# Kernel optimization log

Hardware: AMD Instinct MI355X
Metric: run time of the kernel (lower is better)

The kernel has to match this reference:

```python
import jax, jax.numpy as jnp
import numpy as np

N_NODES = 50000
N_EDGES = 600000
NUM_ENTITIES = 50000
EMBED = 128
HIDDEN = 128
NUM_TYPES = 16


def setup_inputs() -> dict:
    key = jax.random.key(0)
    ks = jax.random.split(key, 12)
    entity = jax.random.randint(ks[0], (N_NODES,), 0, NUM_ENTITIES, dtype=jnp.int64 if jax.config.jax_enable_x64 else jnp.int32)
    edge_index = jax.random.randint(ks[1], (2, N_EDGES), 0, N_NODES, dtype=jnp.int32)
    s = 1.0 / np.sqrt(EMBED)
    emb = jax.random.normal(ks[2], (NUM_ENTITIES, EMBED), jnp.float32)
    emb = emb.at[0].set(0.0)  # padding_idx=0
    W1_l = jax.random.uniform(ks[3], (EMBED, HIDDEN), jnp.float32, -s, s)
    b1 = jax.random.uniform(ks[4], (HIDDEN,), jnp.float32, -s, s)
    W1_r = jax.random.uniform(ks[5], (EMBED, HIDDEN), jnp.float32, -s, s)
    W2_l = jax.random.uniform(ks[6], (HIDDEN, HIDDEN), jnp.float32, -s, s)
    b2 = jax.random.uniform(ks[7], (HIDDEN,), jnp.float32, -s, s)
    W2_r = jax.random.uniform(ks[8], (HIDDEN, HIDDEN), jnp.float32, -s, s)
    Wc = jax.random.uniform(ks[9], (HIDDEN, NUM_TYPES), jnp.float32, -s, s)
    bc = jax.random.uniform(ks[10], (NUM_TYPES,), jnp.float32, -s, s)
    return {"entity": entity, "edge_index": edge_index, "emb": emb,
            "W1_l": W1_l, "b1": b1, "W1_r": W1_r,
            "W2_l": W2_l, "b2": b2, "W2_r": W2_r,
            "Wc": Wc, "bc": bc}


def _sage_conv(x, src, dst, Wl, bl, Wr):
    # PyG SAGEConv (aggr='mean'): out = lin_l(mean_{j->i} x_j) + lin_r(x_i)
    msgs = x[src]                                            # [E, D] gather
    agg = jax.ops.segment_sum(msgs, dst, num_segments=N_NODES)
    deg = jax.ops.segment_sum(jnp.ones((src.shape[0],), x.dtype), dst, num_segments=N_NODES)
    agg = agg / jnp.maximum(deg, 1.0)[:, None]               # mean; 0 for isolated nodes
    return agg @ Wl + bl + x @ Wr


def reference(entity, edge_index, emb, W1_l, b1, W1_r, W2_l, b2, W2_r, Wc, bc):
    src, dst = edge_index[0], edge_index[1]
    x = emb[entity]                                          # [N, 128] embedding lookup
    x = jax.nn.relu(_sage_conv(x, src, dst, W1_l, b1, W1_r))
    x = _sage_conv(x, src, dst, W2_l, b2, W2_r)
    return x @ Wc + bc                                       # [N, num_node_types]
```

## Files before the change

kernel.cpp:

```cpp
#include <hip/hip_runtime.h>

typedef _Float16 half4  __attribute__((ext_vector_type(4)));
typedef _Float16 half8  __attribute__((ext_vector_type(8)));
typedef float    f32x4  __attribute__((ext_vector_type(4)));

#define EC 768
#define CAP 4096
#define CHUNK 2048
#define CPAD 16

__device__ __forceinline__ void gather_dev(const int* __restrict__ ent,
                                           const float* __restrict__ emb,
                                           _Float16* __restrict__ X, int gb, int N) {
  int t = gb * 256 + threadIdx.x;
  if (t >= N * 16) return;
  int node = t >> 4, g = t & 15;
  const float4* s = (const float4*)(emb + (long)ent[node] * 128 + g * 8);
  float4 a = s[0], c = s[1];
  half8 o;
  o[0] = (_Float16)a.x; o[1] = (_Float16)a.y; o[2] = (_Float16)a.z; o[3] = (_Float16)a.w;
  o[4] = (_Float16)c.x; o[5] = (_Float16)c.y; o[6] = (_Float16)c.z; o[7] = (_Float16)c.w;
  *(half8*)(X + (long)t * 8) = o;
}

__device__ __forceinline__ void pack_dev(const float* Wa, const float* Wb,
                                         _Float16* out, int NT, int ncols, int t) {
  int lane = t & 63, tile = t >> 6;
  int nt = tile % NT, kt = tile / NT;
  int n  = nt * 16 + (lane & 15);
  int kb = kt * 32 + (lane >> 4) * 8;
  half8 o;
#pragma unroll
  for (int j = 0; j < 8; ++j) {
    int k = kb + j;
    float w = (k < 128) ? Wa[k * ncols + n] : Wb[(k - 128) * ncols + n];
    o[j] = (_Float16)w;
  }
  *(half8*)(out + (long)t * 8) = o;
}

__global__ __launch_bounds__(256) void bucketA_k(
    const int* __restrict__ src, const int* __restrict__ dst,
    int* __restrict__ cur, int* __restrict__ buck,
    const int* __restrict__ ent, const float* __restrict__ emb, _Float16* __restrict__ X,
    const float* __restrict__ W1l, const float* __restrict__ W1r, _Float16* __restrict__ Wp1,
    const float* __restrict__ W2l, const float* __restrict__ W2r, const float* __restrict__ Wc,
    _Float16* __restrict__ Wz, const float* __restrict__ b2, const float* __restrict__ bc,
    float* __restrict__ bpr, int N, int E, int NA, int NBUCK, int ST, int IBA) {
  int b = blockIdx.x;
  if (b < IBA) {
    int grp = b / ST, ph = b % ST;
    if (ph != 0) { gather_dev(ent, emb, X, grp * (ST - 1) + ph - 1, N); return; }
    __shared__ int lbin[256], gbase[256];
    int tl = threadIdx.x;
    lbin[tl] = 0; __syncthreads();
    int e0 = grp * CHUNK;
    int pk[8], bn[8], lr[8];
    if (e0 + CHUNK <= E) {
      const int4* dp = (const int4*)(dst + e0 + tl * 8);
      const int4* sp = (const int4*)(src + e0 + tl * 8);
      int4 d0 = dp[0], d1 = dp[1], s0 = sp[0], s1 = sp[1];
      int dv[8] = {d0.x, d0.y, d0.z, d0.w, d1.x, d1.y, d1.z, d1.w};
      int sv[8] = {s0.x, s0.y, s0.z, s0.w, s1.x, s1.y, s1.z, s1.w};
#pragma unroll
      for (int k = 0; k < 8; ++k) {
        bn[k] = dv[k] >> 8;
        pk[k] = (sv[k] << 8) | (dv[k] & 255);
        lr[k] = atomicAdd(&lbin[bn[k]], 1);
      }
    } else {
#pragma unroll
      for (int k = 0; k < 8; ++k) {
        int e = e0 + tl * 8 + k;
        bn[k] = -1;
        if (e < E) {
          int d = dst[e];
          bn[k] = d >> 8;
          pk[k] = (src[e] << 8) | (d & 255);
          lr[k] = atomicAdd(&lbin[bn[k]], 1);
        }
      }
    }
    __syncthreads();
    gbase[tl] = (tl < NBUCK && lbin[tl]) ? atomicAdd(&cur[tl * CPAD], lbin[tl]) : 0;
    __syncthreads();
#pragma unroll
    for (int k = 0; k < 8; ++k) {
      if (bn[k] >= 0) {
        int idx = gbase[bn[k]] + lr[k];
        if (idx < CAP) buck[(long)bn[k] * CAP + idx] = pk[k];
      }
    }
  } else if (b < IBA + 16) {
    pack_dev(W1l, W1r, Wp1, 8, 128, (b - IBA) * 256 + threadIdx.x);
  } else if (b < IBA + 32) {
    int i = (b - IBA - 16) * 256 + threadIdx.x;
    int j = i & 7, lane = (i >> 3) & 63, tile = i >> 9;
    int nt = tile & 1, kt = tile >> 1;
    int k = kt * 32 + (lane >> 4) * 8 + j;
    int c = lane & 15;
    const float* W = nt ? W2r : W2l;
    float s = 0.f;
#pragma unroll 8
    for (int q = 0; q < 128; ++q) s += W[k * 128 + q] * Wc[q * 16 + c];
    Wz[i] = (_Float16)s;
  } else {
    int n = threadIdx.x;
    if (n < 16) {
      float s = bc[n];
      for (int k = 0; k < 128; ++k) s += b2[k] * Wc[k * 16 + n];
      bpr[n] = s;
    }
  }
}

__global__ __launch_bounds__(512) void bucketB_k(
    const int* __restrict__ cur, const int* __restrict__ buck,
    int* __restrict__ row_off, int* __restrict__ csr, int N, int E, int NBUCK) {
  int B0 = blockIdx.x, tl = threadIdx.x;
  __shared__ int sA[256], cnt[256], sB[256], run[256];
  if (tl < 256) sA[tl] = (tl < NBUCK) ? cur[tl * CPAD] : 0;
  if (tl < 256) cnt[tl] = 0;
  __syncthreads();
  for (int off = 1; off < 256; off <<= 1) {
    int a = (tl < 256) ? sA[tl] : 0;
    int bb = (tl >= off && tl < 256) ? sA[tl - off] : 0;
    __syncthreads();
    if (tl < 256) sA[tl] = a + bb;
    __syncthreads();
  }
  int bsz = cur[B0 * CPAD]; if (bsz > CAP) bsz = CAP;
  int ebase = sA[B0] - bsz;
  const int* bp = buck + (long)B0 * CAP;
  for (int i = tl; i < bsz; i += 512) atomicAdd(&cnt[bp[i] & 255], 1);
  __syncthreads();
  int cv = (tl < 256) ? cnt[tl] : 0;
  if (tl < 256) sB[tl] = cv;
  __syncthreads();
  for (int off = 1; off < 256; off <<= 1) {
    int a = (tl < 256) ? sB[tl] : 0;
    int bb = (tl >= off && tl < 256) ? sB[tl - off] : 0;
    __syncthreads();
    if (tl < 256) sB[tl] = a + bb;
    __syncthreads();
  }
  if (tl < 256) {
    int loff = sB[tl] - cv;
    int node = (B0 << 8) + tl;
    if (node < N) row_off[node] = ebase + loff;
    if (B0 == 0 && tl == 0) row_off[N] = E;
    run[tl] = loff;
  }
  __syncthreads();
  for (int i = tl; i < bsz; i += 512) {
    int w = bp[i];
    int r = atomicAdd(&run[w & 255], 1);
    csr[ebase + r] = w >> 8;
  }
}

__device__ __forceinline__ void agg_to_lds(const _Float16* __restrict__ X,
                                           const int* __restrict__ row_off,
                                           const int* __restrict__ csr,
                                           _Float16* ab, int* eidx,
                                           int row0, int M, int lane) {
  int nd_end = min(row0 + 16, M);
  int ebeg = row_off[row0 < M ? row0 : M - 1];
  int eend = row_off[nd_end];
  int cnt  = eend - ebeg;
  bool fits = (cnt <= EC);
  if (fits)
    for (int i = lane; i < cnt; i += 64) eidx[i] = csr[ebeg + i];
  int g = lane >> 4, j = lane & 15;
#pragma unroll
  for (int batch = 0; batch < 4; ++batch) {
    int node = row0 + batch * 4 + g;
    int nc = (node < M) ? node : M - 1;
    int beg = row_off[nc], end = row_off[nc + 1];
    half8 acc = (half8)(_Float16)0.f;
    if (fits) {
      const int* ix = eidx + (beg - ebeg);
      int n = end - beg;
#pragma unroll 8
      for (int e = 0; e < n; ++e) {
        half8 v = *(const half8*)(X + (long)ix[e] * 128 + j * 8);
        acc += v;
      }
    } else {
#pragma unroll 8
      for (int e = beg; e < end; ++e) {
        half8 v = *(const half8*)(X + (long)csr[e] * 128 + j * 8);
        acc += v;
      }
    }
    _Float16 inv = (_Float16)(1.f / fmaxf((float)(end - beg), 1.f));
    acc *= (half8)inv;
    *(half8*)(ab + (batch * 4 + g) * 136 + j * 8) = acc;
  }
}

__global__ __launch_bounds__(128) void gemm1z_k(const _Float16* __restrict__ X,
                                                const int* __restrict__ row_off,
                                                const int* __restrict__ csr,
                                                const _Float16* __restrict__ Bp,
                                                const float* __restrict__ bias,
                                                const _Float16* __restrict__ Bz,
                                                const float* __restrict__ bprime,
                                                _Float16* __restrict__ Zl,
                                                float* __restrict__ Pr, int M) {
  __shared__ _Float16 abuf[2][16 * 136];
  __shared__ int      ebuf[2][EC];
  int wave = threadIdx.x >> 6, lane = threadIdx.x & 63;
  _Float16* ab = abuf[wave];
  int row0 = blockIdx.x * 32 + wave * 16;
  agg_to_lds(X, row_off, csr, ab, ebuf[wave], row0, M, lane);
  int m = lane & 15, quad = lane >> 4;
  int arow = row0 + m; if (arow > M - 1) arow = M - 1;
  f32x4 acc[8];
#pragma unroll
  for (int i = 0; i < 8; ++i) acc[i] = (f32x4){0.f, 0.f, 0.f, 0.f};
#pragma unroll
  for (int kt = 0; kt < 8; ++kt) {
    half8 af = (kt < 4) ? *(const half8*)(ab + m * 136 + kt * 32 + quad * 8)
                        : *(const half8*)(X + (long)arow * 128 + (kt - 4) * 32 + quad * 8);
#pragma unroll
    for (int nt = 0; nt < 8; ++nt) {
      half8 bf = *(const half8*)(Bp + ((long)(kt * 8 + nt) * 64 + lane) * 8);
      acc[nt] = __builtin_amdgcn_mfma_f32_16x16x32_f16(af, bf, acc[nt], 0, 0, 0);
    }
  }
#pragma unroll
  for (int nt = 0; nt < 8; ++nt) {
    float bv = bias[nt * 16 + m];
#pragma unroll
    for (int r = 0; r < 4; ++r)
      ab[(quad * 4 + r) * 136 + nt * 16 + m] = (_Float16)fmaxf(acc[nt][r] + bv, 0.f);
  }
  f32x4 a0 = (f32x4){0.f, 0.f, 0.f, 0.f}, a1 = a0;
#pragma unroll
  for (int kt = 0; kt < 4; ++kt) {
    half8 af = *(const half8*)(ab + m * 136 + kt * 32 + quad * 8);
    half8 b0 = *(const half8*)(Bz + ((long)(kt * 2 + 0) * 64 + lane) * 8);
    half8 b1 = *(const half8*)(Bz + ((long)(kt * 2 + 1) * 64 + lane) * 8);
    a0 = __builtin_amdgcn_mfma_f32_16x16x32_f16(af, b0, a0, 0, 0, 0);
    a1 = __builtin_amdgcn_mfma_f32_16x16x32_f16(af, b1, a1, 0, 0, 0);
  }
  float bv = bprime[m];
#pragma unroll
  for (int r = 0; r < 4; ++r) {
    int orow = row0 + quad * 4 + r;
    if (orow < M) {
      Zl[(long)orow * 16 + m] = (_Float16)a0[r];
      Pr[(long)orow * 16 + m] = a1[r] + bv;
    }
  }
}

__global__ __launch_bounds__(256) void aggout_k(const _Float16* __restrict__ Zl,
                                                const float* __restrict__ Pr,
                                                const int* __restrict__ row_off,
                                                const int* __restrict__ csr,
                                                float* __restrict__ out, int M) {
  int t = blockIdx.x * 256 + threadIdx.x;
  int node = t >> 2, q = t & 3;
  if (node >= M) return;
  int beg = row_off[node], end = row_off[node + 1];
  float a0 = 0.f, a1 = 0.f, a2 = 0.f, a3 = 0.f;
#pragma unroll 8
  for (int e = beg; e < end; ++e) {
    half4 v = *(const half4*)(Zl + (long)csr[e] * 16 + q * 4);
    a0 += (float)v[0]; a1 += (float)v[1]; a2 += (float)v[2]; a3 += (float)v[3];
  }
  float inv = 1.f / fmaxf((float)(end - beg), 1.f);
  long o = (long)node * 16 + q * 4;
  const float4 pv = *(const float4*)(Pr + o);
  float4 ov;
  ov.x = a0 * inv + pv.x; ov.y = a1 * inv + pv.y;
  ov.z = a2 * inv + pv.z; ov.w = a3 * inv + pv.w;
  *(float4*)(out + o) = ov;
}

extern "C" void kernel_launch(void* const* d_in, const int* in_sizes, int n_in,
                              void* d_out, int out_size, void* d_ws, size_t ws_size,
                              hipStream_t stream) {
  const int N = in_sizes[0];
  const int E = in_sizes[1] / 2;
  const int*   entity = (const int*)d_in[0];
  const int*   e_src  = (const int*)d_in[1];
  const int*   e_dst  = e_src + E;
  const float* emb    = (const float*)d_in[2];
  const float* W1l    = (const float*)d_in[3];
  const float* b1     = (const float*)d_in[4];
  const float* W1r    = (const float*)d_in[5];
  const float* W2l    = (const float*)d_in[6];
  const float* b2     = (const float*)d_in[7];
  const float* W2r    = (const float*)d_in[8];
  const float* Wc     = (const float*)d_in[9];
  const float* bc     = (const float*)d_in[10];
  float* out = (float*)d_out;

  const int NBUCK = (N + 255) >> 8;

  char* p = (char*)d_ws;
  _Float16* x0  = (_Float16*)p; p += (size_t)N * 128 * 2;
  _Float16* Wp1 = (_Float16*)p; p += 256 * 128 * 2;
  _Float16* Wz  = (_Float16*)p; p += 128 * 32 * 2;
  float*    bpr = (float*)p;    p += 16 * 4;
  _Float16* Zl  = (_Float16*)p; p += (size_t)N * 16 * 2;
  float*    Pr  = (float*)p;    p += (size_t)N * 16 * 4;
  int* cur     = (int*)p; p += (size_t)NBUCK * CPAD * 4;
  int* row_off = (int*)p; p += (size_t)(N + 1) * 4;
  int* csr     = (int*)p; p += (size_t)E * 4;
  int* buck    = (int*)p; p += (size_t)NBUCK * CAP * 4;

  const int NA = (E + CHUNK - 1) / CHUNK;
  const int GB = (N * 16 + 255) / 256;
  const int GAper = (GB + NA - 1) / NA;
  const int ST  = GAper + 1;
  const int IBA = ST * NA;

  hipMemsetAsync(cur, 0, (size_t)NBUCK * CPAD * 4, stream);

  bucketA_k<<<IBA + 33, 256, 0, stream>>>(e_src, e_dst, cur, buck,
                                          entity, emb, x0, W1l, W1r, Wp1,
                                          W2l, W2r, Wc, Wz, b2, bc, bpr,
                                          N, E, NA, NBUCK, ST, IBA);
  bucketB_k<<<NBUCK, 512, 0, stream>>>(cur, buck, row_off, csr, N, E, NBUCK);
  gemm1z_k<<<(N + 31) / 32, 128, 0, stream>>>(x0, row_off, csr, Wp1, b1,
                                              Wz, bpr, Zl, Pr, N);
  aggout_k<<<(N * 4 + 255) / 256, 256, 0, stream>>>(Zl, Pr, row_off, csr, out, N);
}
```

Baseline: 162.4 us.

## Split embedding gather between bucketA and bucketB kernels to balance load

Caps the gather work co-scheduled with edge bucketing in the first kernel at four units per bucketing block. The remaining gather units move into extra blocks appended to the CSR-building kernel, which otherwise launches only a few hundred blocks. The aim is to shorten the first kernel and fill idle compute units during the second. The risk is that the extra blocks contend with the bucket blocks for bandwidth or delay them.

```diff
diff --git a/kernel.cpp b/kernel.cpp
--- a/kernel.cpp
+++ b/kernel.cpp
@@ -8,11 +8,13 @@
 #define CAP 4096
 #define CHUNK 2048
 #define CPAD 16
-
-__device__ __forceinline__ void gather_dev(const int* __restrict__ ent,
-                                           const float* __restrict__ emb,
-                                           _Float16* __restrict__ X, int gb, int N) {
-  int t = gb * 256 + threadIdx.x;
+#define GA_PER 4
+
+__device__ __forceinline__ void gather_unit(const int* __restrict__ ent,
+                                            const float* __restrict__ emb,
+                                            _Float16* __restrict__ X,
+                                            int unit, int lt, int N) {
+  int t = unit * 256 + lt;
   if (t >= N * 16) return;
   int node = t >> 4, g = t & 15;
   const float4* s = (const float4*)(emb + (long)ent[node] * 128 + g * 8);
@@ -46,11 +48,11 @@
     const float* __restrict__ W1l, const float* __restrict__ W1r, _Float16* __restrict__ Wp1,
     const float* __restrict__ W2l, const float* __restrict__ W2r, const float* __restrict__ Wc,
     _Float16* __restrict__ Wz, const float* __restrict__ b2, const float* __restrict__ bc,
-    float* __restrict__ bpr, int N, int E, int NA, int NBUCK, int ST, int IBA) {
+    float* __restrict__ bpr, int N, int E, int NA, int NBUCK, int IBA) {
   int b = blockIdx.x;
   if (b < IBA) {
-    int grp = b / ST, ph = b % ST;
-    if (ph != 0) { gather_dev(ent, emb, X, grp * (ST - 1) + ph - 1, N); return; }
+    int grp = b / (GA_PER + 1), ph = b % (GA_PER + 1);
+    if (ph != 0) { gather_unit(ent, emb, X, grp * GA_PER + ph - 1, threadIdx.x, N); return; }
     __shared__ int lbin[256], gbase[256];
     int tl = threadIdx.x;
     lbin[tl] = 0; __syncthreads();
@@ -116,8 +118,15 @@
 
 __global__ __launch_bounds__(512) void bucketB_k(
     const int* __restrict__ cur, const int* __restrict__ buck,
-    int* __restrict__ row_off, int* __restrict__ csr, int N, int E, int NBUCK) {
+    int* __restrict__ row_off, int* __restrict__ csr,
+    const int* __restrict__ ent, const float* __restrict__ emb,
+    _Float16* __restrict__ X, int goff, int N, int E, int NBUCK) {
   int B0 = blockIdx.x, tl = threadIdx.x;
+  if (B0 >= NBUCK) {
+    int unit = goff + (B0 - NBUCK) * 2 + (tl >> 8);
+    gather_unit(ent, emb, X, unit, tl & 255, N);
+    return;
+  }
   __shared__ int sA[256], cnt[256], sB[256], run[256];
   if (tl < 256) sA[tl] = (tl < NBUCK) ? cur[tl * CPAD] : 0;
   if (tl < 256) cnt[tl] = 0;
@@ -313,19 +322,21 @@
   int* csr     = (int*)p; p += (size_t)E * 4;
   int* buck    = (int*)p; p += (size_t)NBUCK * CAP * 4;
 
-  const int NA = (E + CHUNK - 1) / CHUNK;
-  const int GB = (N * 16 + 255) / 256;
-  const int GAper = (GB + NA - 1) / NA;
-  const int ST  = GAper + 1;
-  const int IBA = ST * NA;
+  const int NA  = (E + CHUNK - 1) / CHUNK;
+  const int GB  = (N * 16 + 255) / 256;
+  const int IBA = (GA_PER + 1) * NA;
+  int G1 = NA * GA_PER; if (G1 > GB) G1 = GB;
+  const int G2 = GB - G1;
+  const int BG = (G2 + 1) / 2;
 
   hipMemsetAsync(cur, 0, (size_t)NBUCK * CPAD * 4, stream);
 
   bucketA_k<<<IBA + 33, 256, 0, stream>>>(e_src, e_dst, cur, buck,
                                           entity, emb, x0, W1l, W1r, Wp1,
                                           W2l, W2r, Wc, Wz, b2, bc, bpr,
-                                          N, E, NA, NBUCK, ST, IBA);
-  bucketB_k<<<NBUCK, 512, 0, stream>>>(cur, buck, row_off, csr, N, E, NBUCK);
+                                          N, E, NA, NBUCK, IBA);
+  bucketB_k<<<NBUCK + BG, 512, 0, stream>>>(cur, buck, row_off, csr,
+                                            entity, emb, x0, G1, N, E, NBUCK);
   gemm1z_k<<<(N + 31) / 32, 128, 0, stream>>>(x0, row_off, csr, Wp1, b1,
                                               Wz, bpr, Zl, Pr, N);
   aggout_k<<<(N * 4 + 255) / 256, 256, 0, stream>>>(Zl, Pr, row_off, csr, out, N);
```

New measurement: 155.8 us, median of 3. 4.0% less time.
